# Performance work log

Hardware: AMD Instinct MI355X
Metric: run time of the kernel (lower is better)

Reference implementation:

```python
import jax, jax.numpy as jnp
import numpy as np

BETA = 0.5
THR = 1.0

@jax.custom_vjp
def spike(u):
    # heaviside fire; surrogate ATan gradient (snntorch default, alpha=2)
    return (u > 0.0).astype(u.dtype)

def _spike_fwd(u):
    return spike(u), u

def _spike_bwd(u, g):
    return (g / (1.0 + (jnp.pi * u) ** 2),)

spike.defvjp(_spike_fwd, _spike_bwd)

def setup_inputs() -> dict:
    key = jax.random.key(0)
    k = jax.random.split(key, 5)
    T, B, NI, NH, NO = 100, 65536, 2, 10, 4
    x = jax.random.normal(k[0], (T, B, NI), dtype=jnp.float32)
    # PyTorch Linear init: U(-1/sqrt(fan_in), 1/sqrt(fan_in))
    W1 = jax.random.uniform(k[1], (NH, NI), jnp.float32, -1/np.sqrt(NI), 1/np.sqrt(NI))
    b1 = jax.random.uniform(k[2], (NH,), jnp.float32, -1/np.sqrt(NI), 1/np.sqrt(NI))
    W2 = jax.random.uniform(k[3], (NO, NH), jnp.float32, -1/np.sqrt(NH), 1/np.sqrt(NH))
    b2 = jax.random.uniform(k[4], (NO,), jnp.float32, -1/np.sqrt(NH), 1/np.sqrt(NH))
    return {"x": x, "W1": W1, "b1": b1, "W2": W2, "b2": b2}

def _lif(mem_prev, syn):
    # snntorch Leaky, reset_mechanism='subtract':
    # reset computed from PRE-update membrane, detached
    reset = jax.lax.stop_gradient((mem_prev > THR).astype(syn.dtype))
    mem = BETA * mem_prev + syn - reset * THR
    spk = spike(mem - THR)
    return spk, mem

def reference(x, W1, b1, W2, b2):
    T, B = x.shape[0], x.shape[1]
    mem1_0 = jnp.zeros((B, W1.shape[0]), x.dtype)
    mem2_0 = jnp.zeros((B, W2.shape[0]), x.dtype)

    def step(carry, xt):
        mem1, mem2 = carry
        syn1 = xt @ W1.T + b1            # [B, NH]
        spk1, mem1 = _lif(mem1, syn1)
        syn2 = spk1 @ W2.T + b2          # [B, NO]
        spk2, mem2 = _lif(mem2, syn2)
        return (mem1, mem2), (spk1, mem1, spk2, mem2)

    _, (spk1_rec, mem1_rec, spk2_rec, mem2_rec) = jax.lax.scan(step, (mem1_0, mem2_0), x)
    return spk1_rec, mem1_rec, spk2_rec, mem2_rec
```

## Files before the change

### kernel.cpp

```cpp
#include <hip/hip_runtime.h>
#include <stdint.h>

#define T_STEPS 100
#define BATCH   65536
#define NI      2
#define NH      10
#define NO      4
#define KCH     10
#define TC      10

typedef float vf2 __attribute__((ext_vector_type(2)));
typedef float vf4 __attribute__((ext_vector_type(4)));

__device__ __forceinline__ float uload(const float* p) {
    return __uint_as_float((uint32_t)__builtin_amdgcn_readfirstlane((int)__float_as_uint(*p)));
}

#define LOAD_WEIGHTS                                                        \
    float w1[NH][NI], bb1[NH], w2[NO][NH], bb2[NO];                         \
    _Pragma("unroll") for (int h = 0; h < NH; ++h) {                        \
        w1[h][0] = uload(&W1[h * NI + 0]);                                  \
        w1[h][1] = uload(&W1[h * NI + 1]);                                  \
        bb1[h]   = uload(&b1[h]);                                           \
    }                                                                       \
    _Pragma("unroll") for (int o = 0; o < NO; ++o) {                        \
        _Pragma("unroll") for (int h = 0; h < NH; ++h)                      \
            w2[o][h] = uload(&W2[o * NH + h]);                              \
        bb2[o] = uload(&b2[o]);                                             \
    }

__device__ __forceinline__ void lif_step(
    const float x0, const float x1,
    const float w1[NH][NI], const float bb1[NH],
    const float w2[NO][NH], const float bb2[NO],
    float m1[NH], float m2[NO], float spk1[NH], float spk2[NO])
{
#pragma unroll
    for (int h = 0; h < NH; ++h) {
        float syn   = __builtin_fmaf(x1, w1[h][1], x0 * w1[h][0]) + bb1[h];
        float reset = (m1[h] > 1.0f) ? 1.0f : 0.0f;
        float m     = 0.5f * m1[h] + syn;
        m           = m - reset;
        m1[h]       = m;
        spk1[h]     = ((m - 1.0f) > 0.0f) ? 1.0f : 0.0f;
    }
#pragma unroll
    for (int o = 0; o < NO; ++o) {
        float acc = spk1[0] * w2[o][0];
#pragma unroll
        for (int h = 1; h < NH; ++h) acc = __builtin_fmaf(spk1[h], w2[o][h], acc);
        float syn   = acc + bb2[o];
        float reset = (m2[o] > 1.0f) ? 1.0f : 0.0f;
        float m     = 0.5f * m2[o] + syn;
        m           = m - reset;
        m2[o]       = m;
        spk2[o]     = ((m - 1.0f) > 0.0f) ? 1.0f : 0.0f;
    }
}

__global__ __launch_bounds__(256, 4) void snn_all(
    const float* __restrict__ x, const float* __restrict__ W1,
    const float* __restrict__ b1, const float* __restrict__ W2,
    const float* __restrict__ b2, float* __restrict__ out)
{
    LOAD_WEIGHTS;

    const int tid  = threadIdx.x;
    const int k    = blockIdx.x % KCH;
    const int bb   = blockIdx.x / KCH;
    const int b    = bb * 256 + tid;
    const int w    = tid >> 6;
    const int lane = tid & 63;
    const int wb0  = bb * 256 + (w << 6);

    const size_t sec = (size_t)T_STEPS * BATCH;
    float* o_spk1 = out;
    float* o_mem1 = out + sec * NH;
    float* o_spk2 = out + 2 * sec * NH;
    float* o_mem2 = out + 2 * sec * NH + sec * NO;

    const vf2* xp = (const vf2*)x + b;
    vf2 xb[TC];
#pragma unroll
    for (int j = 0; j < TC; ++j) xb[j] = xp[(size_t)j * BATCH];

    float m1[NH], m2[NO];
#pragma unroll
    for (int h = 0; h < NH; ++h) m1[h] = 0.0f;
#pragma unroll
    for (int o = 0; o < NO; ++o) m2[o] = 0.0f;

    for (int tt = 0; tt < k * TC; tt += TC) {
#pragma unroll
        for (int j = 0; j < TC; ++j) {
            float spk1[NH], spk2[NO];
            lif_step(xb[j].x, xb[j].y, w1, bb1, w2, bb2, m1, m2, spk1, spk2);
            xb[j] = xp[(size_t)(tt + TC + j) * BATCH];
        }
    }

    __shared__ vf4 stage[4][2][160];
    float* s_spk = (float*)&stage[w][0][0];
    float* s_mem = (float*)&stage[w][1][0];

#pragma unroll
    for (int j = 0; j < TC; ++j) {
        const int t = k * TC + j;
        float spk1[NH], spk2[NO];
        lif_step(xb[j].x, xb[j].y, w1, bb1, w2, bb2, m1, m2, spk1, spk2);

        {
            vf2* qs = (vf2*)s_spk;
            vf2* qm = (vf2*)s_mem;
#pragma unroll
            for (int i = 0; i < NH / 2; ++i) {
                vf2 vs; vs.x = spk1[2 * i]; vs.y = spk1[2 * i + 1];
                vf2 vm; vm.x = m1[2 * i];   vm.y = m1[2 * i + 1];
                qs[lane * 5 + i] = vs;
                qm[lane * 5 + i] = vm;
            }
        }
        __builtin_amdgcn_wave_barrier();

        {
            float* g = o_spk1 + (size_t)t * BATCH * NH + (size_t)wb0 * NH;
            vf4* g4 = (vf4*)g;
            g4[lane]      = stage[w][0][lane];
            g4[64 + lane] = stage[w][0][64 + lane];
            ((vf2*)g)[256 + lane] = ((vf2*)s_spk)[256 + lane];
        }
        {
            float* g = o_mem1 + (size_t)t * BATCH * NH + (size_t)wb0 * NH;
            vf4* g4 = (vf4*)g;
            g4[lane]      = stage[w][1][lane];
            g4[64 + lane] = stage[w][1][64 + lane];
            ((vf2*)g)[256 + lane] = ((vf2*)s_mem)[256 + lane];
        }
        __builtin_amdgcn_wave_barrier();

        {
            vf4 vs; vs.x = spk2[0]; vs.y = spk2[1]; vs.z = spk2[2]; vs.w = spk2[3];
            vf4 vm; vm.x = m2[0];   vm.y = m2[1];   vm.z = m2[2];   vm.w = m2[3];
            *(vf4*)(o_spk2 + ((size_t)t * BATCH + b) * NO) = vs;
            *(vf4*)(o_mem2 + ((size_t)t * BATCH + b) * NO) = vm;
        }
    }
}

extern "C" void kernel_launch(void* const* d_in, const int* in_sizes, int n_in,
                              void* d_out, int out_size, void* d_ws, size_t ws_size,
                              hipStream_t stream) {
    const float* x  = (const float*)d_in[0];
    const float* W1 = (const float*)d_in[1];
    const float* b1 = (const float*)d_in[2];
    const float* W2 = (const float*)d_in[3];
    const float* b2 = (const float*)d_in[4];
    float* out = (float*)d_out;

    snn_all<<<(BATCH / 256) * KCH, 256, 0, stream>>>(x, W1, b1, W2, b2, out);
}
```

Measured before the change: 882.6 us.

## Halve time chunks and batch output staging across groups of four steps

Reduces the number of time chunks per batch tile from 10 to 5, cutting the redundant prefix recomputation each block performs to reach its chunk. Output writes are staged in larger shared buffers covering four steps at once, and input x is double-buffered with a two-group prefetch. The trade-off is half as many blocks, a larger shared-memory footprint and a lower launch-bounds occupancy target, which reduces latency hiding.

```diff
diff --git a/kernel.cpp b/kernel.cpp
--- a/kernel.cpp
+++ b/kernel.cpp
@@ -6,8 +6,10 @@
 #define NI      2
 #define NH      10
 #define NO      4
-#define KCH     10
-#define TC      10
+#define KCH     5
+#define TC      20
+#define GS      4
+#define GPC     (TC / GS)
 
 typedef float vf2 __attribute__((ext_vector_type(2)));
 typedef float vf4 __attribute__((ext_vector_type(4)));
@@ -58,7 +60,7 @@
     }
 }
 
-__global__ __launch_bounds__(256, 4) void snn_all(
+__global__ __launch_bounds__(256, 2) void snn_fused(
     const float* __restrict__ x, const float* __restrict__ W1,
     const float* __restrict__ b1, const float* __restrict__ W2,
     const float* __restrict__ b2, float* __restrict__ out)
@@ -80,9 +82,6 @@
     float* o_mem2 = out + 2 * sec * NH + sec * NO;
 
     const vf2* xp = (const vf2*)x + b;
-    vf2 xb[TC];
-#pragma unroll
-    for (int j = 0; j < TC; ++j) xb[j] = xp[(size_t)j * BATCH];
 
     float m1[NH], m2[NO];
 #pragma unroll
@@ -90,59 +89,84 @@
 #pragma unroll
     for (int o = 0; o < NO; ++o) m2[o] = 0.0f;
 
-    for (int tt = 0; tt < k * TC; tt += TC) {
+    const int Gscan = k * GPC;
+    const int G     = Gscan + GPC;
+
+    vf2 xc[GS], xn[GS];
 #pragma unroll
-        for (int j = 0; j < TC; ++j) {
-            float spk1[NH], spk2[NO];
-            lif_step(xb[j].x, xb[j].y, w1, bb1, w2, bb2, m1, m2, spk1, spk2);
-            xb[j] = xp[(size_t)(tt + TC + j) * BATCH];
+    for (int i = 0; i < GS; ++i) xc[i] = xp[(size_t)i * BATCH];
+#pragma unroll
+    for (int i = 0; i < GS; ++i) xn[i] = xp[(size_t)(GS + i) * BATCH];
+
+    __shared__ float sA[GS][256][NH];
+    __shared__ float sB[GS][256][NH];
+
+    vf4 s2r[GS], m2r[GS];
+
+    for (int g = 0; g < G; ++g) {
+        if (g < Gscan) {
+#pragma unroll
+            for (int j = 0; j < GS; ++j) {
+                float spk1[NH], spk2[NO];
+                lif_step(xc[j].x, xc[j].y, w1, bb1, w2, bb2, m1, m2, spk1, spk2);
+            }
+        } else {
+#pragma unroll
+            for (int j = 0; j < GS; ++j) {
+                float spk1[NH], spk2[NO];
+                lif_step(xc[j].x, xc[j].y, w1, bb1, w2, bb2, m1, m2, spk1, spk2);
+                vf2* qa = (vf2*)&sA[j][tid][0];
+                vf2* qb = (vf2*)&sB[j][tid][0];
+#pragma unroll
+                for (int i = 0; i < NH / 2; ++i) {
+                    vf2 vs; vs.x = spk1[2 * i]; vs.y = spk1[2 * i + 1];
+                    vf2 vm; vm.x = m1[2 * i];   vm.y = m1[2 * i + 1];
+                    qa[i] = vs;
+                    qb[i] = vm;
+                }
+                vf4 v2; v2.x = spk2[0]; v2.y = spk2[1]; v2.z = spk2[2]; v2.w = spk2[3];
+                vf4 vm2; vm2.x = m2[0]; vm2.y = m2[1]; vm2.z = m2[2]; vm2.w = m2[3];
+                s2r[j] = v2;
+                m2r[j] = vm2;
+            }
+            __builtin_amdgcn_wave_barrier();
+
+            const int t0g = k * TC + (g - Gscan) * GS;
+#pragma unroll
+            for (int j = 0; j < GS; ++j) {
+                const int t = t0g + j;
+                {
+                    const float* ls = &sA[j][w * 64][0];
+                    vf4 r0 = ((const vf4*)ls)[lane];
+                    vf4 r1 = ((const vf4*)ls)[64 + lane];
+                    vf2 r2 = ((const vf2*)ls)[256 + lane];
+                    float* gd = o_spk1 + ((size_t)t * BATCH + wb0) * NH;
+                    ((vf4*)gd)[lane]      = r0;
+                    ((vf4*)gd)[64 + lane] = r1;
+                    ((vf2*)gd)[256 + lane] = r2;
+                }
+                {
+                    const float* ls = &sB[j][w * 64][0];
+                    vf4 r0 = ((const vf4*)ls)[lane];
+                    vf4 r1 = ((const vf4*)ls)[64 + lane];
+                    vf2 r2 = ((const vf2*)ls)[256 + lane];
+                    float* gd = o_mem1 + ((size_t)t * BATCH + wb0) * NH;
+                    ((vf4*)gd)[lane]      = r0;
+                    ((vf4*)gd)[64 + lane] = r1;
+                    ((vf2*)gd)[256 + lane] = r2;
+                }
+                *(vf4*)(o_spk2 + ((size_t)t * BATCH + b) * NO) = s2r[j];
+                *(vf4*)(o_mem2 + ((size_t)t * BATCH + b) * NO) = m2r[j];
+            }
+            __builtin_amdgcn_wave_barrier();
         }
-    }
-
-    __shared__ vf4 stage[4][2][160];
-    float* s_spk = (float*)&stage[w][0][0];
-    float* s_mem = (float*)&stage[w][1][0];
 
 #pragma unroll
-    for (int j = 0; j < TC; ++j) {
-        const int t = k * TC + j;
-        float spk1[NH], spk2[NO];
-        lif_step(xb[j].x, xb[j].y, w1, bb1, w2, bb2, m1, m2, spk1, spk2);
-
-        {
-            vf2* qs = (vf2*)s_spk;
-            vf2* qm = (vf2*)s_mem;
+        for (int i = 0; i < GS; ++i) xc[i] = xn[i];
+        if (g + 2 < G) {
 #pragma unroll
-            for (int i = 0; i < NH / 2; ++i) {
-                vf2 vs; vs.x = spk1[2 * i]; vs.y = spk1[2 * i + 1];
-                vf2 vm; vm.x = m1[2 * i];   vm.y = m1[2 * i + 1];
-                qs[lane * 5 + i] = vs;
-                qm[lane * 5 + i] = vm;
-            }
-        }
-        __builtin_amdgcn_wave_barrier();
-
-        {
-            float* g = o_spk1 + (size_t)t * BATCH * NH + (size_t)wb0 * NH;
-            vf4* g4 = (vf4*)g;
-            g4[lane]      = stage[w][0][lane];
-            g4[64 + lane] = stage[w][0][64 + lane];
-            ((vf2*)g)[256 + lane] = ((vf2*)s_spk)[256 + lane];
-        }
-        {
-            float* g = o_mem1 + (size_t)t * BATCH * NH + (size_t)wb0 * NH;
-            vf4* g4 = (vf4*)g;
-            g4[lane]      = stage[w][1][lane];
-            g4[64 + lane] = stage[w][1][64 + lane];
-            ((vf2*)g)[256 + lane] = ((vf2*)s_mem)[256 + lane];
-        }
-        __builtin_amdgcn_wave_barrier();
-
-        {
-            vf4 vs; vs.x = spk2[0]; vs.y = spk2[1]; vs.z = spk2[2]; vs.w = spk2[3];
-            vf4 vm; vm.x = m2[0];   vm.y = m2[1];   vm.z = m2[2];   vm.w = m2[3];
-            *(vf4*)(o_spk2 + ((size_t)t * BATCH + b) * NO) = vs;
-            *(vf4*)(o_mem2 + ((size_t)t * BATCH + b) * NO) = vm;
+            for (int i = 0; i < GS; ++i)
+                xn[i] = xp[(size_t)((g + 2) * GS + i) * BATCH];
         }
     }
 }
@@ -157,5 +181,5 @@
     const float* b2 = (const float*)d_in[4];
     float* out = (float*)d_out;
 
-    snn_all<<<(BATCH / 256) * KCH, 256, 0, stream>>>(x, W1, b1, W2, b2, out);
+    snn_fused<<<(BATCH / 256) * KCH, 256, 0, stream>>>(x, W1, b1, W2, b2, out);
 }
```

Result: faster. 795.6 us (-9.9%).
